# Kernel tuning notes

Measured on AMD Instinct MI355X. Metric: run time of the kernel, lower is better.

## Reference

```python
import jax, jax.numpy as jnp
import numpy as np

STAGE = 100  # number of weight bins


def _bin_reconstruct(w, affine):
    # Faithful vectorization of the 100-iter binning loop: element in bin i
    # (half-open interval) gets scaled by affine[i]; the max element falls
    # outside every bin (w < wmin + stage*range/stage fails) and is zeroed.
    flat = w.reshape(-1)
    wmin, wmax = flat.min(), flat.max()
    idx = jnp.floor((flat - wmin) / (wmax - wmin) * STAGE).astype(jnp.int32)
    mask = (idx < STAGE).astype(flat.dtype)  # mask is detached in torch (non-diff anyway)
    scale = affine[jnp.clip(idx, 0, STAGE - 1)]
    return flat * scale * mask


def _kl_vs_laplace(new_flat, lap):
    # F.kl_div(log_softmax(w), softmax(lap), reduction='none').mean()
    logq = jax.nn.log_softmax(new_flat)
    p = jax.nn.softmax(lap)
    return (p * (jnp.log(p) - logq)).mean()


def _adder2d(x, w, stride, padding, groups=1):
    # AdderNet conv: out = -sum_k |patch_k - w_k| (no bias)
    O, Cg, kh, kw = w.shape
    patches = jax.lax.conv_general_dilated_patches(
        x, (kh, kw), (stride, stride), [(padding, padding), (padding, padding)])
    B, _, Hp, Wp = patches.shape  # channel dim ordered (C, kh, kw), C-major
    if groups == 1:
        p = patches.reshape(B, 1, Cg * kh * kw, Hp, Wp)
        wf = w.reshape(1, O, Cg * kh * kw, 1, 1)
    else:  # depthwise: groups == C_in, Cg == 1, O == C_in
        p = patches.reshape(B, O, kh * kw, Hp, Wp)
        wf = w.reshape(1, O, kh * kw, 1, 1)
    return -jnp.abs(p - wf).sum(axis=2)  # [B, O, Hp, Wp]


def _bn_train(x, g, b, eps=1e-5):
    # BatchNorm2d in training mode (batch statistics, biased variance)
    m = x.mean(axis=(0, 2, 3), keepdims=True)
    v = ((x - m) ** 2).mean(axis=(0, 2, 3), keepdims=True)
    return (x - m) * jax.lax.rsqrt(v + eps) * g.reshape(1, -1, 1, 1) + b.reshape(1, -1, 1, 1)


def _forward(x, sw_ds, sw_c1, sw_c2, sw_c3, a_ds, a_c1, a_c2, a_c3, peg_w,
             g1, b1, g2, b2, g3, b3, gds, bds, lap_ds, lap_c1, lap_c2, lap_c3):
    kl = jnp.float32(0.0)
    f_ds = _bin_reconstruct(sw_ds, a_ds)
    kl = kl + _kl_vs_laplace(f_ds, lap_ds)
    f_c1 = _bin_reconstruct(sw_c1, a_c1)
    kl = kl + _kl_vs_laplace(f_c1, lap_c1)
    residual = jax.nn.relu(_bn_train(_adder2d(x, f_ds.reshape(sw_ds.shape), 1, 0), gds, bds))
    h = _adder2d(x, f_c1.reshape(sw_c1.shape), 1, 0)
    h = _adder2d(h, peg_w, 1, 1, groups=peg_w.shape[0])  # PEG depthwise 3x3
    h = jax.nn.relu(_bn_train(h, g1, b1))
    f_c2 = _bin_reconstruct(sw_c2, a_c2)
    kl = kl + _kl_vs_laplace(f_c2, lap_c2)
    h = _adder2d(h, f_c2.reshape(sw_c2.shape), 1, 1)
    h = jax.nn.relu(_bn_train(h, g2, b2))
    f_c3 = _bin_reconstruct(sw_c3, a_c3)
    kl = kl + _kl_vs_laplace(f_c3, lap_c3)
    h = _adder2d(h, f_c3.reshape(sw_c3.shape), 1, 0)
    h = _bn_train(h, g3, b3)  # bn3 gamma zero-initialized
    return jax.nn.relu(h + residual), kl


def setup_inputs() -> dict:
    key = jax.random.key(0)
    ks = jax.random.split(key, 16)
    inp = {
        'x': jax.random.normal(ks[0], (4, 128, 28, 28), jnp.float32),
        'sw_downsample': jax.random.normal(ks[1], (256, 128, 1, 1), jnp.float32) * 0.05,
        'sw_conv1': jax.random.normal(ks[2], (64, 128, 1, 1), jnp.float32) * 0.05,
        'sw_conv2': jax.random.normal(ks[3], (64, 64, 3, 3), jnp.float32) * 0.05,
        'sw_conv3': jax.random.normal(ks[4], (256, 64, 1, 1), jnp.float32) * 0.05,
        'downsample_affine': jax.random.normal(ks[5], (100,), jnp.float32),
        'conv1_affine': jax.random.normal(ks[6], (100,), jnp.float32),
        'conv2_affine': jax.random.normal(ks[7], (100,), jnp.float32),
        'conv3_affine': jax.random.normal(ks[8], (100,), jnp.float32),
        'peg_w': jax.random.normal(ks[9], (64, 1, 3, 3), jnp.float32) * 0.05,
        'bn1_g': jnp.ones((64,), jnp.float32), 'bn1_b': jnp.zeros((64,), jnp.float32),
        'bn2_g': jnp.ones((64,), jnp.float32), 'bn2_b': jnp.zeros((64,), jnp.float32),
        'bn3_g': jnp.zeros((256,), jnp.float32), 'bn3_b': jnp.zeros((256,), jnp.float32),
        'bnds_g': jnp.ones((256,), jnp.float32), 'bnds_b': jnp.zeros((256,), jnp.float32),
        # Laplace(0, 2) samples, drawn once in setup so the reference is deterministic
        'lap_ds': jax.random.laplace(ks[10], (32768,), jnp.float32) * 2.0,
        'lap_c1': jax.random.laplace(ks[11], (8192,), jnp.float32) * 2.0,
        'lap_c2': jax.random.laplace(ks[12], (36864,), jnp.float32) * 2.0,
        'lap_c3': jax.random.laplace(ks[13], (16384,), jnp.float32) * 2.0,
    }
    return inp


def reference(x, sw_downsample, sw_conv1, sw_conv2, sw_conv3,
              downsample_affine, conv1_affine, conv2_affine, conv3_affine, peg_w,
              bn1_g, bn1_b, bn2_g, bn2_b, bn3_g, bn3_b, bnds_g, bnds_b,
              lap_ds, lap_c1, lap_c2, lap_c3):
    return _forward(x, sw_downsample, sw_conv1, sw_conv2, sw_conv3,
                    downsample_affine, conv1_affine, conv2_affine, conv3_affine, peg_w,
                    bn1_g, bn1_b, bn2_g, bn2_b, bn3_g, bn3_b, bnds_g, bnds_b,
                    lap_ds, lap_c1, lap_c2, lap_c3)
```

## Files before the change

### kernel.cpp

```cpp
#include <hip/hip_runtime.h>
#include <math.h>


#define HW 784
#define NB 4
#define STAGE 100

__device__ __forceinline__ float wredSum(float v){
  for (int o = 32; o > 0; o >>= 1) v += __shfl_down(v, o, 64);
  return v;
}
__device__ __forceinline__ float wredMax(float v){
  for (int o = 32; o > 0; o >>= 1) v = fmaxf(v, __shfl_down(v, o, 64));
  return v;
}
__device__ __forceinline__ float wredMin(float v){
  for (int o = 32; o > 0; o >>= 1) v = fminf(v, __shfl_down(v, o, 64));
  return v;
}
__device__ __forceinline__ double wredSumD(double v){
  for (int o = 32; o > 0; o >>= 1) v += __shfl_down(v, o, 64);
  return v;
}

__device__ float blockMin4(float v){
  __shared__ float shn[4];
  __syncthreads();
  v = wredMin(v);
  if ((threadIdx.x & 63) == 0) shn[threadIdx.x >> 6] = v;
  __syncthreads();
  return fminf(fminf(shn[0], shn[1]), fminf(shn[2], shn[3]));
}
__device__ float blockMax4(float v){
  __shared__ float shx[4];
  __syncthreads();
  v = wredMax(v);
  if ((threadIdx.x & 63) == 0) shx[threadIdx.x >> 6] = v;
  __syncthreads();
  return fmaxf(fmaxf(shx[0], shx[1]), fmaxf(shx[2], shx[3]));
}

__device__ void stats4(float v0, float v1, float v2, float v3,
                       double* sumP, double* sqP, int oc0){
  __shared__ double sred[4][8];
  __syncthreads();
  const int w = threadIdx.x >> 6;
  float vv[4] = {v0, v1, v2, v3};
  #pragma unroll
  for (int i = 0; i < 4; i++){
    double d = (double)vv[i];
    double s = wredSumD(d);
    double q = wredSumD(d * d);
    if ((threadIdx.x & 63) == 0){ sred[w][i] = s; sred[w][4 + i] = q; }
  }
  __syncthreads();
  if (threadIdx.x < 8){
    double tot = sred[0][threadIdx.x] + sred[1][threadIdx.x]
               + sred[2][threadIdx.x] + sred[3][threadIdx.x];
    int i = threadIdx.x & 3;
    if (threadIdx.x < 4) atomicAdd(&sumP[oc0 + i], tot);
    else                 atomicAdd(&sqP[oc0 + i],  tot);
  }
}
__device__ void stats2(float v0, float v1, double* sumP, double* sqP, int oc0){
  __shared__ double sred2[4][4];
  __syncthreads();
  const int w = threadIdx.x >> 6;
  float vv[2] = {v0, v1};
  #pragma unroll
  for (int i = 0; i < 2; i++){
    double d = (double)vv[i];
    double s = wredSumD(d);
    double q = wredSumD(d * d);
    if ((threadIdx.x & 63) == 0){ sred2[w][i] = s; sred2[w][2 + i] = q; }
  }
  __syncthreads();
  if (threadIdx.x < 4){
    double tot = sred2[0][threadIdx.x] + sred2[1][threadIdx.x]
               + sred2[2][threadIdx.x] + sred2[3][threadIdx.x];
    int i = threadIdx.x & 1;
    if (threadIdx.x < 2) atomicAdd(&sumP[oc0 + i], tot);
    else                 atomicAdd(&sqP[oc0 + i],  tot);
  }
}

__device__ void klAccum(float se, float sel, float sef, float sq, double* dst){
  __shared__ double kls[4][4];
  __syncthreads();
  const int w = threadIdx.x >> 6;
  double a0 = wredSumD((double)se);
  double a1 = wredSumD((double)sel);
  double a2 = wredSumD((double)sef);
  double a3 = wredSumD((double)sq);
  if ((threadIdx.x & 63) == 0){
    kls[w][0] = a0; kls[w][1] = a1; kls[w][2] = a2; kls[w][3] = a3;
  }
  __syncthreads();
  if (threadIdx.x < 4){
    double tot = kls[0][threadIdx.x] + kls[1][threadIdx.x]
               + kls[2][threadIdx.x] + kls[3][threadIdx.x];
    atomicAdd(&dst[threadIdx.x], tot);
  }
}

__device__ __forceinline__ float reconv(float vv, float mn, float rng,
                                        const float* saff){
  float q = (vv - mn) / rng * 100.0f;
  int idx = (int)floorf(q);
  float nv = 0.0f;
  if (idx < STAGE){
    int ci = idx < 0 ? 0 : (idx > STAGE - 1 ? STAGE - 1 : idx);
    nv = vv * saff[ci];
  }
  return nv;
}

__device__ __forceinline__ void mmReduce(const float* mmbuf, int tens,
                                         float& mn, float& mx){
  mn = 3.402823466e38f; mx = -3.402823466e38f;
  #pragma unroll
  for (int k = 0; k < 16; k++){
    mn = fminf(mn, mmbuf[tens * 32 + k]);
    mx = fmaxf(mx, mmbuf[tens * 32 + 16 + k]);
  }
}

__global__ __launch_bounds__(256) void minmax_kernel(
    const float* w0, int n0, const float* w1, int n1,
    const float* w2, int n2, const float* w3, int n3,
    float* mmbuf, double* dstat)
{
  if (threadIdx.x < 21) dstat[blockIdx.x * 21 + threadIdx.x] = 0.0;
  const int tens = blockIdx.x >> 4, slot = blockIdx.x & 15;
  const float* w; int n;
  if      (tens == 0){ w = w0; n = n0; }
  else if (tens == 1){ w = w1; n = n1; }
  else if (tens == 2){ w = w2; n = n2; }
  else               { w = w3; n = n3; }
  float mn = 3.402823466e38f, mx = -3.402823466e38f;
  for (int i = slot * 256 + threadIdx.x; i < n; i += 4096){
    float v = w[i];
    mn = fminf(mn, v); mx = fmaxf(mx, v);
  }
  mn = blockMin4(mn); mx = blockMax4(mx);
  if (threadIdx.x == 0){
    mmbuf[tens * 32 + slot]      = mn;
    mmbuf[tens * 32 + 16 + slot] = mx;
  }
}

__global__ __launch_bounds__(256) void front_kernel(
    const float* __restrict__ x,
    const float* __restrict__ w_ds, const float* __restrict__ aff_ds,
    const float* __restrict__ lap_ds,
    const float* __restrict__ w_c1, const float* __restrict__ aff_c1,
    const float* __restrict__ lap_c1,
    const float* __restrict__ w_c2, const float* __restrict__ aff_c2,
    const float* __restrict__ lap_c2, float* __restrict__ f_c2,
    const float* __restrict__ w_c3, const float* __restrict__ aff_c3,
    const float* __restrict__ lap_c3,
    const float* __restrict__ peg_w, const float* __restrict__ mmbuf,
    float* __restrict__ A, float* __restrict__ T2b, double* __restrict__ dS)
{
  const int t = threadIdx.x;
  if (blockIdx.x < 512){
    const int a = blockIdx.x;
    const int chunk = a & 3, og = (a >> 2) & 31, b = a >> 7;
    const int oc0 = og * 8;
    __shared__ float saff[STAGE];
    __shared__ float sw[1024];
    if (t < STAGE) saff[t] = aff_ds[t];
    float mn, mx; mmReduce(mmbuf, 0, mn, mx);
    const float rng = mx - mn;
    __syncthreads();
    for (int k = t; k < 1024; k += 256)
      sw[k] = reconv(w_ds[oc0 * 128 + k], mn, rng, saff);
    __syncthreads();

    const int px = chunk * 196 + t;
    float v0=0,v1=0,v2=0,v3=0,v4=0,v5=0,v6=0,v7=0;
    if (t < 196){
      const float* xp = x + (size_t)b * 128 * HW + px;
      float c0=0,c1=0,c2=0,c3=0,c4=0,c5=0,c6=0,c7=0;
      #pragma unroll 4
      for (int c = 0; c < 128; c++){
        float xv = xp[(size_t)c * HW];
        c0 += fabsf(xv - sw[c]);
        c1 += fabsf(xv - sw[128 + c]);
        c2 += fabsf(xv - sw[256 + c]);
        c3 += fabsf(xv - sw[384 + c]);
        c4 += fabsf(xv - sw[512 + c]);
        c5 += fabsf(xv - sw[640 + c]);
        c6 += fabsf(xv - sw[768 + c]);
        c7 += fabsf(xv - sw[896 + c]);
      }
      v0=-c0; v1=-c1; v2=-c2; v3=-c3; v4=-c4; v5=-c5; v6=-c6; v7=-c7;
      float* op = A + ((size_t)(b * 256 + oc0)) * HW + px;
      op[0]=v0; op[HW]=v1; op[2*HW]=v2; op[3*HW]=v3;
      op[4*HW]=v4; op[5*HW]=v5; op[6*HW]=v6; op[7*HW]=v7;
    }
    stats4(v0, v1, v2, v3, dS + 0, dS + 256, oc0);
    stats4(v4, v5, v6, v7, dS + 0, dS + 256, oc0 + 4);

    if (b == 0 && chunk == 0){
      float se = 0, sel = 0, sef = 0, sq = 0;
      for (int k = t; k < 1024; k += 256){
        float l = lap_ds[oc0 * 128 + k];
        float e = expf(l);
        se += e; sel += e * l; sef += e * sw[k];
        sq += expf(sw[k]);
      }
      klAccum(se, sel, sef, sq, dS + 1280 + 0);
    }
  } else if (blockIdx.x < 768){
    const int a = blockIdx.x - 512;
    const int rc = a & 3, og = (a >> 2) & 15, b = a >> 6;
    const int oc0 = og * 4;
    __shared__ float saffc[STAGE];
    __shared__ float swc[512];
    __shared__ float swp[36];
    __shared__ float sT1[4][256];
    if (t < STAGE) saffc[t] = aff_c1[t];
    if (t >= 128 && t < 164) swp[t - 128] = peg_w[oc0 * 9 + (t - 128)];
    float mn, mx; mmReduce(mmbuf, 1, mn, mx);
    const float rng = mx - mn;
    __syncthreads();
    for (int k = t; k < 512; k += 256)
      swc[k] = reconv(w_c1[oc0 * 128 + k], mn, rng, saffc);

    {
      float* tb = T2b + (size_t)(b * 64 + oc0) * 960;
      for (int i = t; i < 112; i += 256){
        int ch = i / 28;
        int j  = i - ch * 28;
        int r7 = j >> 2, cs = j & 3;
        int col = (cs == 0) ? 0 : 28 + cs;
        tb[(size_t)ch * 960 + (rc * 7 + 1 + r7) * 32 + col] = 0.0f;
      }
      if (rc == 0){
        for (int i = t; i < 128; i += 256){
          int ch = i >> 5, col = i & 31;
          tb[(size_t)ch * 960 + col] = 0.0f;
        }
      }
      if (rc == 3){
        for (int i = t; i < 128; i += 256){
          int ch = i >> 5, col = i & 31;
          tb[(size_t)ch * 960 + 29 * 32 + col] = 0.0f;
        }
      }
    }
    __syncthreads();

    if (t < 252){
      const int rr = t / 28;
      const int col = t - rr * 28;
      const int wr = rc * 7 - 1 + rr;
      float tv0 = 0, tv1 = 0, tv2 = 0, tv3 = 0;
      if (wr >= 0 && wr < 28){
        const float* xp = x + (size_t)b * 128 * HW + wr * 28 + col;
        float c0 = 0, c1 = 0, c2 = 0, c3 = 0;
        #pragma unroll 4
        for (int c = 0; c < 128; c++){
          float xv = xp[(size_t)c * HW];
          c0 += fabsf(xv - swc[c]);
          c1 += fabsf(xv - swc[128 + c]);
          c2 += fabsf(xv - swc[256 + c]);
          c3 += fabsf(xv - swc[384 + c]);
        }
        tv0 = -c0; tv1 = -c1; tv2 = -c2; tv3 = -c3;
      }
      sT1[0][t] = tv0; sT1[1][t] = tv1; sT1[2][t] = tv2; sT1[3][t] = tv3;
    }
    __syncthreads();
    float v0 = 0, v1 = 0, v2 = 0, v3 = 0;
    if (t < 196){
      const int r = t / 28, col = t - r * 28;
      float c0 = 0, c1 = 0, c2 = 0, c3 = 0;
      #pragma unroll
      for (int ky = 0; ky < 3; ky++){
        #pragma unroll
        for (int kx = 0; kx < 3; kx++){
          int cc = col + kx - 1;
          bool ok = (cc >= 0) && (cc < 28);
          int idx = ok ? ((r + ky) * 28 + cc) : 0;
          float p0 = ok ? sT1[0][idx] : 0.0f;
          float p1 = ok ? sT1[1][idx] : 0.0f;
          float p2 = ok ? sT1[2][idx] : 0.0f;
          float p3 = ok ? sT1[3][idx] : 0.0f;
          int wk = ky * 3 + kx;
          c0 += fabsf(p0 - swp[wk]);
          c1 += fabsf(p1 - swp[9 + wk]);
          c2 += fabsf(p2 - swp[18 + wk]);
          c3 += fabsf(p3 - swp[27 + wk]);
        }
      }
      v0 = -c0; v1 = -c1; v2 = -c2; v3 = -c3;
      const int prow = rc * 7 + r + 1;
      float* op = T2b + (size_t)(b * 64 + oc0) * 960 + prow * 32 + (col + 1);
      op[0] = v0; op[960] = v1; op[1920] = v2; op[2880] = v3;
    }
    stats4(v0, v1, v2, v3, dS + 512, dS + 576, oc0);

    if (b == 0 && rc == 0){
      float se = 0, sel = 0, sef = 0, sq = 0;
      for (int k = t; k < 512; k += 256){
        float l = lap_c1[oc0 * 128 + k];
        float e = expf(l);
        se += e; sel += e * l; sef += e * swc[k];
        sq += expf(swc[k]);
      }
      klAccum(se, sel, sef, sq, dS + 1280 + 4);
    }
  } else if (blockIdx.x < 832){
    const int j = blockIdx.x - 768;
    __shared__ float saff2[STAGE];
    if (t < STAGE) saff2[t] = aff_c2[t];
    float mn, mx; mmReduce(mmbuf, 2, mn, mx);
    const float rng = mx - mn;
    __syncthreads();
    float se = 0, sel = 0, sef = 0, sq = 0;
    for (int k = t; k < 576; k += 256){
      float nv = reconv(w_c2[j * 576 + k], mn, rng, saff2);
      f_c2[j * 576 + k] = nv;
      float l = lap_c2[j * 576 + k];
      float e = expf(l);
      se += e; sel += e * l; sef += e * nv; sq += expf(nv);
    }
    klAccum(se, sel, sef, sq, dS + 1280 + 8);
  } else {
    const int j = blockIdx.x - 832;
    __shared__ float saff3[STAGE];
    if (t < STAGE) saff3[t] = aff_c3[t];
    float mn, mx; mmReduce(mmbuf, 3, mn, mx);
    const float rng = mx - mn;
    __syncthreads();
    float se = 0, sel = 0, sef = 0, sq = 0;
    for (int k = t; k < 1024; k += 256){
      float nv = reconv(w_c3[j * 1024 + k], mn, rng, saff3);
      float l = lap_c3[j * 1024 + k];
      float e = expf(l);
      se += e; sel += e * l; sef += e * nv; sq += expf(nv);
    }
    klAccum(se, sel, sef, sq, dS + 1280 + 12);
  }
}

__global__ __launch_bounds__(256) void mid3x3_kernel(
    const float* __restrict__ T2b, const float* __restrict__ f_c2,
    const float* __restrict__ g1, const float* __restrict__ b1,
    float* __restrict__ T3, double* __restrict__ dS)
{
  const int t = threadIdx.x;
  const int a = blockIdx.x;
  const int chunk = a & 3, og = (a >> 2) & 31, b = a >> 7;
  const int oc0 = og * 2;
  __shared__ float sT[64 * 288];
  __shared__ float ssc[64], ssb[64];

  if (t < 64){
    double s  = dS[512 + t] * (1.0 / 3136.0);
    double vr = dS[576 + t] * (1.0 / 3136.0) - s * s;
    float scale = g1[t] * rsqrtf((float)vr + 1e-5f);
    ssc[t] = scale; ssb[t] = b1[t] - (float)s * scale;
  }
  __syncthreads();

  const float* src = T2b + (size_t)b * 64 * 960 + chunk * 224;
  float4* s4 = (float4*)sT;
  #pragma unroll
  for (int q = 0; q < 18; q++){
    int flat = q * 256 + t;
    int c = flat / 72;
    int w = flat - c * 72;
    float4 v = *(const float4*)(src + (size_t)c * 960 + w * 4);
    int rr = w >> 3;
    int prow = chunk * 7 + rr;
    bool rok = (prow >= 1) && (prow <= 28);
    int pc0 = (w & 7) * 4;
    float sc = ssc[c], sb = ssb[c];
    v.x = (rok && pc0     >= 1 && pc0     <= 28) ? fmaxf(v.x * sc + sb, 0.f) : 0.f;
    v.y = (rok && pc0 + 1 >= 1 && pc0 + 1 <= 28) ? fmaxf(v.y * sc + sb, 0.f) : 0.f;
    v.z = (rok && pc0 + 2 >= 1 && pc0 + 2 <= 28) ? fmaxf(v.z * sc + sb, 0.f) : 0.f;
    v.w = (rok && pc0 + 3 >= 1 && pc0 + 3 <= 28) ? fmaxf(v.w * sc + sb, 0.f) : 0.f;
    s4[flat] = v;
  }
  __syncthreads();

  const float* __restrict__ wA = f_c2 + oc0 * 576;
  const float* __restrict__ wB = wA + 576;
  float v0 = 0.0f, v1 = 0.0f;
  if (t < 196){
    const int r = t / 28, col = t - r * 28;
    const float* pbase = sT + r * 32 + col;
    float c0 = 0.0f, c1 = 0.0f;
    #pragma unroll 4
    for (int c = 0; c < 64; c++){
      const float* p = pbase + c * 288;
      float t0 = p[0],  t1 = p[1],  t2 = p[2];
      float t3 = p[32], t4 = p[33], t5 = p[34];
      float t6 = p[64], t7 = p[65], t8 = p[66];
      const float* wa = wA + c * 9;
      const float* wb = wB + c * 9;
      c0 += fabsf(t0 - wa[0]) + fabsf(t1 - wa[1]) + fabsf(t2 - wa[2])
          + fabsf(t3 - wa[3]) + fabsf(t4 - wa[4]) + fabsf(t5 - wa[5])
          + fabsf(t6 - wa[6]) + fabsf(t7 - wa[7]) + fabsf(t8 - wa[8]);
      c1 += fabsf(t0 - wb[0]) + fabsf(t1 - wb[1]) + fabsf(t2 - wb[2])
          + fabsf(t3 - wb[3]) + fabsf(t4 - wb[4]) + fabsf(t5 - wb[5])
          + fabsf(t6 - wb[6]) + fabsf(t7 - wb[7]) + fabsf(t8 - wb[8]);
    }
    v0 = -c0; v1 = -c1;
    const int px = chunk * 196 + t;
    T3[((size_t)(b * 64 + oc0)) * HW + px]     = v0;
    T3[((size_t)(b * 64 + oc0 + 1)) * HW + px] = v1;
  }
  stats2(v0, v1, dS + 640, dS + 704, oc0);
}

__global__ __launch_bounds__(256) void back_kernel(
    const float* __restrict__ T3, const float* __restrict__ w_c3,
    const float* __restrict__ aff_c3, const float* __restrict__ mmbuf,
    const float* __restrict__ g2, const float* __restrict__ b2,
    float* __restrict__ out, double* __restrict__ dS)
{
  const int t = threadIdx.x;
  const int a = blockIdx.x;
  const int chunk = a & 3, og = (a >> 2) & 63, b = a >> 8;
  const int oc0 = og * 4;
  __shared__ float ssc[64], ssb[64], sw[256], saff[STAGE];
  if (t < 64){
    double s  = dS[640 + t] * (1.0 / 3136.0);
    double vr = dS[704 + t] * (1.0 / 3136.0) - s * s;
    float scale = g2[t] * rsqrtf((float)vr + 1e-5f);
    ssc[t] = scale; ssb[t] = b2[t] - (float)s * scale;
  }
  if (t >= 128 && t < 128 + STAGE) saff[t - 128] = aff_c3[t - 128];
  float mn, mx; mmReduce(mmbuf, 3, mn, mx);
  const float rng = mx - mn;
  __syncthreads();
  sw[t] = reconv(w_c3[oc0 * 64 + t], mn, rng, saff);
  __syncthreads();

  const int px = chunk * 196 + t;
  float v0 = 0, v1 = 0, v2 = 0, v3 = 0;
  if (t < 196){
    const float* bp = T3 + (size_t)b * 64 * HW + px;
    float c0 = 0, c1 = 0, c2 = 0, c3 = 0;
    #pragma unroll 4
    for (int c = 0; c < 64; c++){
      float raw = bp[(size_t)c * HW];
      float vv = fmaxf(raw * ssc[c] + ssb[c], 0.0f);
      c0 += fabsf(vv - sw[c]);
      c1 += fabsf(vv - sw[64 + c]);
      c2 += fabsf(vv - sw[128 + c]);
      c3 += fabsf(vv - sw[192 + c]);
    }
    v0 = -c0; v1 = -c1; v2 = -c2; v3 = -c3;
    float* op = out + ((size_t)(b * 256 + oc0)) * HW + px;
    op[0] = v0; op[HW] = v1; op[2 * HW] = v2; op[3 * HW] = v3;
  }
  stats4(v0, v1, v2, v3, dS + 768, dS + 1024, oc0);
}

__global__ __launch_bounds__(256) void final_kernel(
    float* __restrict__ out, const float* __restrict__ A,
    const float* __restrict__ g3, const float* __restrict__ b3,
    const float* __restrict__ gds, const float* __restrict__ bds,
    const double* __restrict__ dS)
{
  __shared__ float s3c[256], s3b[256], sdc[256], sdb[256];
  const int t = threadIdx.x;
  {
    double s  = dS[768 + t] * (1.0 / 3136.0);
    double vr = dS[1024 + t] * (1.0 / 3136.0) - s * s;
    float scale = g3[t] * rsqrtf((float)vr + 1e-5f);
    s3c[t] = scale; s3b[t] = b3[t] - (float)s * scale;
    s  = dS[t] * (1.0 / 3136.0);
    vr = dS[256 + t] * (1.0 / 3136.0) - s * s;
    scale = gds[t] * rsqrtf((float)vr + 1e-5f);
    sdc[t] = scale; sdb[t] = bds[t] - (float)s * scale;
  }
  __syncthreads();
  #pragma unroll
  for (int k = 0; k < 4; k++){
    int n = blockIdx.x * 1024 + k * 256 + t;
    int c = (n / HW) & 255;
    float h = out[n], aa = A[n];
    float r = fmaxf(aa * sdc[c] + sdb[c], 0.0f);
    out[n] = fmaxf(h * s3c[c] + s3b[c] + r, 0.0f);
  }
  if (blockIdx.x == 0 && t == 0){
    const int ns[4] = {32768, 8192, 36864, 16384};
    float kl = 0.0f;
    #pragma unroll
    for (int q = 0; q < 4; q++){
      double se  = dS[1280 + q * 4];
      double sel = dS[1280 + q * 4 + 1];
      double sef = dS[1280 + q * 4 + 2];
      double sq  = dS[1280 + q * 4 + 3];
      kl += (float)((((sel - sef) / se) - log(se) + log(sq)) / (double)ns[q]);
    }
    out[802816] = kl;
  }
}

extern "C" void kernel_launch(void* const* d_in, const int* in_sizes, int n_in,
                              void* d_out, int out_size, void* d_ws, size_t ws_size,
                              hipStream_t stream)
{
  const float* x      = (const float*)d_in[0];
  const float* sw_ds  = (const float*)d_in[1];
  const float* sw_c1  = (const float*)d_in[2];
  const float* sw_c2  = (const float*)d_in[3];
  const float* sw_c3  = (const float*)d_in[4];
  const float* a_ds   = (const float*)d_in[5];
  const float* a_c1   = (const float*)d_in[6];
  const float* a_c2   = (const float*)d_in[7];
  const float* a_c3   = (const float*)d_in[8];
  const float* peg_w  = (const float*)d_in[9];
  const float* bn1_g  = (const float*)d_in[10];
  const float* bn1_b  = (const float*)d_in[11];
  const float* bn2_g  = (const float*)d_in[12];
  const float* bn2_b  = (const float*)d_in[13];
  const float* bn3_g  = (const float*)d_in[14];
  const float* bn3_b  = (const float*)d_in[15];
  const float* bnds_g = (const float*)d_in[16];
  const float* bnds_b = (const float*)d_in[17];
  const float* lap_ds = (const float*)d_in[18];
  const float* lap_c1 = (const float*)d_in[19];
  const float* lap_c2 = (const float*)d_in[20];
  const float* lap_c3 = (const float*)d_in[21];

  float* ws    = (float*)d_ws;
  float* f_c2  = ws;
  float* mmbuf = ws + 36864;
  double* dstat= (double*)(ws + 37120);
  float* A     = ws + 39808;
  float* T3    = ws + 842624;
  float* T2b   = ws + 1043328;

  float* out = (float*)d_out;

  minmax_kernel<<<64, 256, 0, stream>>>(
      sw_ds, 32768, sw_c1, 8192, sw_c2, 36864, sw_c3, 16384, mmbuf, dstat);

  front_kernel<<<848, 256, 0, stream>>>(
      x, sw_ds, a_ds, lap_ds, sw_c1, a_c1, lap_c1,
      sw_c2, a_c2, lap_c2, f_c2, sw_c3, a_c3, lap_c3,
      peg_w, mmbuf, A, T2b, dstat);

  mid3x3_kernel<<<512, 256, 0, stream>>>(T2b, f_c2, bn1_g, bn1_b, T3, dstat);

  back_kernel<<<1024, 256, 0, stream>>>(T3, sw_c3, a_c3, mmbuf,
                                        bn2_g, bn2_b, out, dstat);

  final_kernel<<<784, 256, 0, stream>>>(out, A, bn3_g, bn3_b, bnds_g, bnds_b,
                                        dstat);
}
```

Measured before the change: 170.1 us.

## Register-tile two pixels per thread with vectorized loads in adder convs

The downsample 1x1 adder conv and back_kernel now have each thread compute two adjacent pixels for 4 output channels. They use float2 global loads and float4 shared-memory weight loads, and per-pixel sums and squares are pre-combined before a new stats4p reduction. back_kernel's grid is halved to 512 blocks and the downsample part remaps its block-to-work assignment. final_kernel now handles one float4 per thread. The aim is to cut shared-memory and global load instructions per FLOP and improve memory coalescing, at the cost of fewer threads in flight and more register pressure.

```diff
diff --git a/kernel.cpp b/kernel.cpp
--- a/kernel.cpp
+++ b/kernel.cpp
@@ -6,10 +6,6 @@
 #define NB 4
 #define STAGE 100
 
-__device__ __forceinline__ float wredSum(float v){
-  for (int o = 32; o > 0; o >>= 1) v += __shfl_down(v, o, 64);
-  return v;
-}
 __device__ __forceinline__ float wredMax(float v){
   for (int o = 32; o > 0; o >>= 1) v = fmaxf(v, __shfl_down(v, o, 64));
   return v;
@@ -57,6 +53,26 @@
   if (threadIdx.x < 8){
     double tot = sred[0][threadIdx.x] + sred[1][threadIdx.x]
                + sred[2][threadIdx.x] + sred[3][threadIdx.x];
+    int i = threadIdx.x & 3;
+    if (threadIdx.x < 4) atomicAdd(&sumP[oc0 + i], tot);
+    else                 atomicAdd(&sqP[oc0 + i],  tot);
+  }
+}
+__device__ void stats4p(const double* s, const double* q,
+                        double* sumP, double* sqP, int oc0){
+  __shared__ double sredp[4][8];
+  __syncthreads();
+  const int w = threadIdx.x >> 6;
+  #pragma unroll
+  for (int i = 0; i < 4; i++){
+    double ss = wredSumD(s[i]);
+    double qq = wredSumD(q[i]);
+    if ((threadIdx.x & 63) == 0){ sredp[w][i] = ss; sredp[w][4 + i] = qq; }
+  }
+  __syncthreads();
+  if (threadIdx.x < 8){
+    double tot = sredp[0][threadIdx.x] + sredp[1][threadIdx.x]
+               + sredp[2][threadIdx.x] + sredp[3][threadIdx.x];
     int i = threadIdx.x & 3;
     if (threadIdx.x < 4) atomicAdd(&sumP[oc0 + i], tot);
     else                 atomicAdd(&sqP[oc0 + i],  tot);
@@ -165,46 +181,64 @@
   const int t = threadIdx.x;
   if (blockIdx.x < 512){
     const int a = blockIdx.x;
-    const int chunk = a & 3, og = (a >> 2) & 31, b = a >> 7;
-    const int oc0 = og * 8;
+    const int chunk = a & 1, og = (a >> 1) & 63, b = a >> 7;
+    const int oc0 = og * 4;
     __shared__ float saff[STAGE];
-    __shared__ float sw[1024];
+    __shared__ __align__(16) float sw[512];
     if (t < STAGE) saff[t] = aff_ds[t];
     float mn, mx; mmReduce(mmbuf, 0, mn, mx);
     const float rng = mx - mn;
     __syncthreads();
-    for (int k = t; k < 1024; k += 256)
+    for (int k = t; k < 512; k += 256)
       sw[k] = reconv(w_ds[oc0 * 128 + k], mn, rng, saff);
     __syncthreads();
 
-    const int px = chunk * 196 + t;
-    float v0=0,v1=0,v2=0,v3=0,v4=0,v5=0,v6=0,v7=0;
+    const int px0 = chunk * 392 + 2 * t;
+    float a0x=0,a0y=0,a1x=0,a1y=0,a2x=0,a2y=0,a3x=0,a3y=0;
     if (t < 196){
-      const float* xp = x + (size_t)b * 128 * HW + px;
-      float c0=0,c1=0,c2=0,c3=0,c4=0,c5=0,c6=0,c7=0;
+      const float* xp = x + (size_t)b * 128 * HW + px0;
       #pragma unroll 4
-      for (int c = 0; c < 128; c++){
-        float xv = xp[(size_t)c * HW];
-        c0 += fabsf(xv - sw[c]);
-        c1 += fabsf(xv - sw[128 + c]);
-        c2 += fabsf(xv - sw[256 + c]);
-        c3 += fabsf(xv - sw[384 + c]);
-        c4 += fabsf(xv - sw[512 + c]);
-        c5 += fabsf(xv - sw[640 + c]);
-        c6 += fabsf(xv - sw[768 + c]);
-        c7 += fabsf(xv - sw[896 + c]);
-      }
-      v0=-c0; v1=-c1; v2=-c2; v3=-c3; v4=-c4; v5=-c5; v6=-c6; v7=-c7;
-      float* op = A + ((size_t)(b * 256 + oc0)) * HW + px;
-      op[0]=v0; op[HW]=v1; op[2*HW]=v2; op[3*HW]=v3;
-      op[4*HW]=v4; op[5*HW]=v5; op[6*HW]=v6; op[7*HW]=v7;
-    }
-    stats4(v0, v1, v2, v3, dS + 0, dS + 256, oc0);
-    stats4(v4, v5, v6, v7, dS + 0, dS + 256, oc0 + 4);
+      for (int c4 = 0; c4 < 32; c4++){
+        const float4 w0 = *(const float4*)&sw[      c4*4];
+        const float4 w1 = *(const float4*)&sw[128 + c4*4];
+        const float4 w2 = *(const float4*)&sw[256 + c4*4];
+        const float4 w3 = *(const float4*)&sw[384 + c4*4];
+        const float2 x0 = *(const float2*)(xp + (size_t)(c4*4+0)*HW);
+        const float2 x1 = *(const float2*)(xp + (size_t)(c4*4+1)*HW);
+        const float2 x2 = *(const float2*)(xp + (size_t)(c4*4+2)*HW);
+        const float2 x3 = *(const float2*)(xp + (size_t)(c4*4+3)*HW);
+        a0x += fabsf(x0.x-w0.x)+fabsf(x1.x-w0.y)+fabsf(x2.x-w0.z)+fabsf(x3.x-w0.w);
+        a0y += fabsf(x0.y-w0.x)+fabsf(x1.y-w0.y)+fabsf(x2.y-w0.z)+fabsf(x3.y-w0.w);
+        a1x += fabsf(x0.x-w1.x)+fabsf(x1.x-w1.y)+fabsf(x2.x-w1.z)+fabsf(x3.x-w1.w);
+        a1y += fabsf(x0.y-w1.x)+fabsf(x1.y-w1.y)+fabsf(x2.y-w1.z)+fabsf(x3.y-w1.w);
+        a2x += fabsf(x0.x-w2.x)+fabsf(x1.x-w2.y)+fabsf(x2.x-w2.z)+fabsf(x3.x-w2.w);
+        a2y += fabsf(x0.y-w2.x)+fabsf(x1.y-w2.y)+fabsf(x2.y-w2.z)+fabsf(x3.y-w2.w);
+        a3x += fabsf(x0.x-w3.x)+fabsf(x1.x-w3.y)+fabsf(x2.x-w3.z)+fabsf(x3.x-w3.w);
+        a3y += fabsf(x0.y-w3.x)+fabsf(x1.y-w3.y)+fabsf(x2.y-w3.z)+fabsf(x3.y-w3.w);
+      }
+      float* op = A + ((size_t)(b * 256 + oc0)) * HW + px0;
+      float2 r;
+      r.x = -a0x; r.y = -a0y; *(float2*)(op         ) = r;
+      r.x = -a1x; r.y = -a1y; *(float2*)(op +     HW) = r;
+      r.x = -a2x; r.y = -a2y; *(float2*)(op + 2 * HW) = r;
+      r.x = -a3x; r.y = -a3y; *(float2*)(op + 3 * HW) = r;
+    }
+    {
+      double s[4], q[4];
+      s[0] = -(double)a0x - (double)a0y;
+      s[1] = -(double)a1x - (double)a1y;
+      s[2] = -(double)a2x - (double)a2y;
+      s[3] = -(double)a3x - (double)a3y;
+      q[0] = (double)a0x*a0x + (double)a0y*a0y;
+      q[1] = (double)a1x*a1x + (double)a1y*a1y;
+      q[2] = (double)a2x*a2x + (double)a2y*a2y;
+      q[3] = (double)a3x*a3x + (double)a3y*a3y;
+      stats4p(s, q, dS + 0, dS + 256, oc0);
+    }
 
     if (b == 0 && chunk == 0){
       float se = 0, sel = 0, sef = 0, sq = 0;
-      for (int k = t; k < 1024; k += 256){
+      for (int k = t; k < 512; k += 256){
         float l = lap_ds[oc0 * 128 + k];
         float e = expf(l);
         se += e; sel += e * l; sef += e * sw[k];
@@ -425,9 +459,12 @@
 {
   const int t = threadIdx.x;
   const int a = blockIdx.x;
-  const int chunk = a & 3, og = (a >> 2) & 63, b = a >> 8;
+  const int chunk = a & 1, og = (a >> 1) & 63, b = a >> 7;
   const int oc0 = og * 4;
-  __shared__ float ssc[64], ssb[64], sw[256], saff[STAGE];
+  __shared__ __align__(16) float ssc[64];
+  __shared__ __align__(16) float ssb[64];
+  __shared__ __align__(16) float sw[256];
+  __shared__ float saff[STAGE];
   if (t < 64){
     double s  = dS[640 + t] * (1.0 / 3136.0);
     double vr = dS[704 + t] * (1.0 / 3136.0) - s * s;
@@ -441,25 +478,54 @@
   sw[t] = reconv(w_c3[oc0 * 64 + t], mn, rng, saff);
   __syncthreads();
 
-  const int px = chunk * 196 + t;
-  float v0 = 0, v1 = 0, v2 = 0, v3 = 0;
+  const int px0 = chunk * 392 + 2 * t;
+  float a0x=0,a0y=0,a1x=0,a1y=0,a2x=0,a2y=0,a3x=0,a3y=0;
   if (t < 196){
-    const float* bp = T3 + (size_t)b * 64 * HW + px;
-    float c0 = 0, c1 = 0, c2 = 0, c3 = 0;
+    const float* bp = T3 + (size_t)b * 64 * HW + px0;
     #pragma unroll 4
-    for (int c = 0; c < 64; c++){
-      float raw = bp[(size_t)c * HW];
-      float vv = fmaxf(raw * ssc[c] + ssb[c], 0.0f);
-      c0 += fabsf(vv - sw[c]);
-      c1 += fabsf(vv - sw[64 + c]);
-      c2 += fabsf(vv - sw[128 + c]);
-      c3 += fabsf(vv - sw[192 + c]);
-    }
-    v0 = -c0; v1 = -c1; v2 = -c2; v3 = -c3;
-    float* op = out + ((size_t)(b * 256 + oc0)) * HW + px;
-    op[0] = v0; op[HW] = v1; op[2 * HW] = v2; op[3 * HW] = v3;
-  }
-  stats4(v0, v1, v2, v3, dS + 768, dS + 1024, oc0);
+    for (int c4 = 0; c4 < 16; c4++){
+      const float4 sc = *(const float4*)&ssc[c4*4];
+      const float4 sb = *(const float4*)&ssb[c4*4];
+      const float4 w0 = *(const float4*)&sw[      c4*4];
+      const float4 w1 = *(const float4*)&sw[ 64 + c4*4];
+      const float4 w2 = *(const float4*)&sw[128 + c4*4];
+      const float4 w3 = *(const float4*)&sw[192 + c4*4];
+      const float2 x0 = *(const float2*)(bp + (size_t)(c4*4+0)*HW);
+      const float2 x1 = *(const float2*)(bp + (size_t)(c4*4+1)*HW);
+      const float2 x2 = *(const float2*)(bp + (size_t)(c4*4+2)*HW);
+      const float2 x3 = *(const float2*)(bp + (size_t)(c4*4+3)*HW);
+      float v0x = fmaxf(x0.x*sc.x+sb.x, 0.f), v0y = fmaxf(x0.y*sc.x+sb.x, 0.f);
+      float v1x = fmaxf(x1.x*sc.y+sb.y, 0.f), v1y = fmaxf(x1.y*sc.y+sb.y, 0.f);
+      float v2x = fmaxf(x2.x*sc.z+sb.z, 0.f), v2y = fmaxf(x2.y*sc.z+sb.z, 0.f);
+      float v3x = fmaxf(x3.x*sc.w+sb.w, 0.f), v3y = fmaxf(x3.y*sc.w+sb.w, 0.f);
+      a0x += fabsf(v0x-w0.x)+fabsf(v1x-w0.y)+fabsf(v2x-w0.z)+fabsf(v3x-w0.w);
+      a0y += fabsf(v0y-w0.x)+fabsf(v1y-w0.y)+fabsf(v2y-w0.z)+fabsf(v3y-w0.w);
+      a1x += fabsf(v0x-w1.x)+fabsf(v1x-w1.y)+fabsf(v2x-w1.z)+fabsf(v3x-w1.w);
+      a1y += fabsf(v0y-w1.x)+fabsf(v1y-w1.y)+fabsf(v2y-w1.z)+fabsf(v3y-w1.w);
+      a2x += fabsf(v0x-w2.x)+fabsf(v1x-w2.y)+fabsf(v2x-w2.z)+fabsf(v3x-w2.w);
+      a2y += fabsf(v0y-w2.x)+fabsf(v1y-w2.y)+fabsf(v2y-w2.z)+fabsf(v3y-w2.w);
+      a3x += fabsf(v0x-w3.x)+fabsf(v1x-w3.y)+fabsf(v2x-w3.z)+fabsf(v3x-w3.w);
+      a3y += fabsf(v0y-w3.x)+fabsf(v1y-w3.y)+fabsf(v2y-w3.z)+fabsf(v3y-w3.w);
+    }
+    float* op = out + ((size_t)(b * 256 + oc0)) * HW + px0;
+    float2 r;
+    r.x = -a0x; r.y = -a0y; *(float2*)(op         ) = r;
+    r.x = -a1x; r.y = -a1y; *(float2*)(op +     HW) = r;
+    r.x = -a2x; r.y = -a2y; *(float2*)(op + 2 * HW) = r;
+    r.x = -a3x; r.y = -a3y; *(float2*)(op + 3 * HW) = r;
+  }
+  {
+    double s[4], q[4];
+    s[0] = -(double)a0x - (double)a0y;
+    s[1] = -(double)a1x - (double)a1y;
+    s[2] = -(double)a2x - (double)a2y;
+    s[3] = -(double)a3x - (double)a3y;
+    q[0] = (double)a0x*a0x + (double)a0y*a0y;
+    q[1] = (double)a1x*a1x + (double)a1y*a1y;
+    q[2] = (double)a2x*a2x + (double)a2y*a2y;
+    q[3] = (double)a3x*a3x + (double)a3y*a3y;
+    stats4p(s, q, dS + 768, dS + 1024, oc0);
+  }
 }
 
 __global__ __launch_bounds__(256) void final_kernel(
@@ -481,13 +547,18 @@
     sdc[t] = scale; sdb[t] = bds[t] - (float)s * scale;
   }
   __syncthreads();
-  #pragma unroll
-  for (int k = 0; k < 4; k++){
-    int n = blockIdx.x * 1024 + k * 256 + t;
-    int c = (n / HW) & 255;
-    float h = out[n], aa = A[n];
-    float r = fmaxf(aa * sdc[c] + sdb[c], 0.0f);
-    out[n] = fmaxf(h * s3c[c] + s3b[c] + r, 0.0f);
+  {
+    const int n4 = blockIdx.x * 256 + t;
+    const int c = (n4 / 196) & 255;
+    float4 h  = *(const float4*)&out[(size_t)n4 * 4];
+    float4 aa = *(const float4*)&A[(size_t)n4 * 4];
+    const float scd = sdc[c], sbd = sdb[c], sc3 = s3c[c], sb3 = s3b[c];
+    float4 o;
+    o.x = fmaxf(h.x * sc3 + sb3 + fmaxf(aa.x * scd + sbd, 0.f), 0.f);
+    o.y = fmaxf(h.y * sc3 + sb3 + fmaxf(aa.y * scd + sbd, 0.f), 0.f);
+    o.z = fmaxf(h.z * sc3 + sb3 + fmaxf(aa.z * scd + sbd, 0.f), 0.f);
+    o.w = fmaxf(h.w * sc3 + sb3 + fmaxf(aa.w * scd + sbd, 0.f), 0.f);
+    *(float4*)&out[(size_t)n4 * 4] = o;
   }
   if (blockIdx.x == 0 && t == 0){
     const int ns[4] = {32768, 8192, 36864, 16384};
@@ -551,8 +622,8 @@
 
   mid3x3_kernel<<<512, 256, 0, stream>>>(T2b, f_c2, bn1_g, bn1_b, T3, dstat);
 
-  back_kernel<<<1024, 256, 0, stream>>>(T3, sw_c3, a_c3, mmbuf,
-                                        bn2_g, bn2_b, out, dstat);
+  back_kernel<<<512, 256, 0, stream>>>(T3, sw_c3, a_c3, mmbuf,
+                                       bn2_g, bn2_b, out, dstat);
 
   final_kernel<<<784, 256, 0, stream>>>(out, A, bn3_g, bn3_b, bnds_g, bnds_b,
                                         dstat);
```

Result: no change. 173.3 us (+1.9%).
